# Kernel optimization log

Measured on AMD Instinct MI355X. Metric: run time of the kernel, lower is better.

Reference implementation:

```python
import jax, jax.numpy as jnp
import numpy as np
from jax import lax

EPS = 1e-5      # InstanceNorm2d default eps
SLOPE = 0.2     # LeakyReLU negative slope
K = 3           # kernel size
PAD = 1


def _conv(x, w, pad=PAD):
    # x: [B,C,H,W], w: [O,I,K,K], stride 1
    return lax.conv_general_dilated(x, w, (1, 1), [(pad, pad), (pad, pad)],
                                    dimension_numbers=('NCHW', 'OIHW', 'NCHW'))


def _instance_norm(x, gamma, beta):
    mu = jnp.mean(x, (2, 3), keepdims=True)
    var = jnp.mean((x - mu) ** 2, (2, 3), keepdims=True)
    xn = (x - mu) * lax.rsqrt(var + EPS)
    return xn * gamma[None, :, None, None] + beta[None, :, None, None]


def _lrelu(x):
    return jnp.where(x >= 0, x, SLOPE * x)


def _deform_conv(x, w_off, b_off, w_def):
    # DCNv2: offsets+mask predicted by a 3x3 conv, then modulated bilinear sampling.
    B, C, H, W = x.shape
    om = _conv(x, w_off) + b_off[None, :, None, None]       # [B, 3*K*K, H, W]
    o1, o2, m = jnp.split(om, 3, axis=1)                    # each [B, K*K, H, W]
    off = jnp.concatenate([o1, o2], axis=1)                 # [B, 2*K*K, H, W]
    dy = off[:, 0::2]                                       # [B, K*K, H, W] y-offsets
    dx = off[:, 1::2]                                       # [B, K*K, H, W] x-offsets
    mask = jax.nn.sigmoid(m)                                # [B, K*K, H, W]

    ky = jnp.repeat(jnp.arange(K), K).astype(x.dtype)       # tap row index per k
    kx = jnp.tile(jnp.arange(K), K).astype(x.dtype)         # tap col index per k
    py = dy + jnp.arange(H, dtype=x.dtype)[None, None, :, None] - PAD + ky[None, :, None, None]
    px = dx + jnp.arange(W, dtype=x.dtype)[None, None, None, :] - PAD + kx[None, :, None, None]

    y0 = jnp.floor(py); x0 = jnp.floor(px)
    ly = py - y0; lx = px - x0
    y0i = y0.astype(jnp.int32); x0i = x0.astype(jnp.int32)

    xf = x.reshape(B, C, H * W)

    def gather(iy, ix):
        valid = ((iy >= 0) & (iy < H) & (ix >= 0) & (ix < W)).astype(x.dtype)
        idx = jnp.clip(iy, 0, H - 1) * W + jnp.clip(ix, 0, W - 1)
        v = jax.vmap(lambda f, i: jnp.take(f, i, axis=-1))(xf, idx)  # [B,C,K*K,H,W]
        return v * valid[:, None]

    samp = (gather(y0i, x0i)         * ((1 - ly) * (1 - lx))[:, None]
          + gather(y0i, x0i + 1)     * ((1 - ly) * lx)[:, None]
          + gather(y0i + 1, x0i)     * (ly * (1 - lx))[:, None]
          + gather(y0i + 1, x0i + 1) * (ly * lx)[:, None])          # [B,C,K*K,H,W]

    wk = w_def.reshape(w_def.shape[0], C, K * K)            # [O,C,K*K]
    return jnp.einsum('ock,bckhw,bkhw->bohw', wk, samp, mask)


def setup_inputs() -> dict:
    key = jax.random.key(0)
    ks = jax.random.split(key, 10)
    B, C, H, W = 4, 128, 96, 96
    x = jax.random.normal(ks[0], (B, C, H, W), jnp.float32)
    g1 = 1.0 + 0.05 * jax.random.normal(ks[1], (C,), jnp.float32)
    b1 = 0.05 * jax.random.normal(ks[2], (C,), jnp.float32)
    g2 = 1.0 + 0.05 * jax.random.normal(ks[3], (C,), jnp.float32)
    b2 = 0.05 * jax.random.normal(ks[4], (C,), jnp.float32)
    w1 = jax.random.normal(ks[5], (C, C, K, K), jnp.float32) * 0.03
    bc1 = 0.01 * jax.random.normal(ks[6], (C,), jnp.float32)
    # offset/mask conv: zero-init in the original; use small random values so the
    # irregular bilinear-sampling path is actually exercised.
    w_off = jax.random.normal(ks[7], (3 * K * K, C, K, K), jnp.float32) * 0.01
    b_off = 0.01 * jax.random.normal(ks[8], (3 * K * K,), jnp.float32)
    w_def = jax.random.normal(ks[9], (C, C, K, K), jnp.float32) * 0.03  # DeformConv has bias=None
    return {"x": x, "g1": g1, "b1": b1, "g2": g2, "b2": b2,
            "w1": w1, "bc1": bc1, "w_off": w_off, "b_off": b_off, "w_def": w_def}


def reference(x, g1, b1, g2, b2, w1, bc1, w_off, b_off, w_def):
    h = _lrelu(_instance_norm(x, g1, b1))
    h = _conv(h, w1) + bc1[None, :, None, None]
    h = _lrelu(_instance_norm(h, g2, b2))
    h = _deform_conv(h, w_off, b_off, w_def)
    return h + x
```

## Files before the change

kernel.cpp:

```cpp
#include <hip/hip_runtime.h>
#include <hip/hip_fp16.h>
#include <math.h>

#define HWN 9216
#define HD 96
#define WD 96

typedef _Float16 h8v __attribute__((ext_vector_type(8)));
typedef float f16x16 __attribute__((ext_vector_type(16)));

__device__ __forceinline__ ushort f2h(float f) {
  return __half_as_ushort(__float2half(f));
}
__device__ __forceinline__ __half2 u2h(unsigned u) {
  return __builtin_bit_cast(__half2, u);
}
__device__ __forceinline__ unsigned h2u(__half2 h) {
  return __builtin_bit_cast(unsigned, h);
}
__device__ __forceinline__ h8v u4h(uint4 v) {
  return __builtin_bit_cast(h8v, v);
}
__device__ __forceinline__ f16x16 mfma32(h8v a, h8v b, f16x16 c) {
  return __builtin_amdgcn_mfma_f32_32x32x16_f16(a, b, c, 0, 0, 0);
}
__device__ __forceinline__ __half2 pkmax2(__half2 a, __half2 b) {
  unsigned r;
  asm("v_pk_max_f16 %0, %1, %2" : "=v"(r) : "v"(h2u(a)), "v"(h2u(b)));
  return u2h(r);
}
__device__ __forceinline__ __half2 lrelu2(__half2 v, __half2 c02) {
  return pkmax2(v, __hmul2(v, c02));
}

__global__ __launch_bounds__(256) void packxt_kernel(
    const float* __restrict__ w1, const float* __restrict__ wdef,
    const float* __restrict__ woff, const float* __restrict__ x,
    ushort* __restrict__ w1p, ushort* __restrict__ wdp, ushort* __restrict__ wofp,
    unsigned* __restrict__ xh, float* __restrict__ partS, float* __restrict__ partQ) {
  __shared__ float tl[128][97];
  int bid = blockIdx.x;
  int t = threadIdx.x;
  if (bid < 162) {
    int i = bid * 256 + t;
    const float* src;
    ushort* dst;
    int CT, CO_real, fi;
    if (i < 18432) { src = w1; dst = w1p; CT = 4; CO_real = 128; fi = i; }
    else if (i < 36864) { src = wdef; dst = wdp; CT = 4; CO_real = 128; fi = i - 18432; }
    else { src = woff; dst = wofp; CT = 1; CO_real = 27; fi = i - 36864; }
    int lane = fi & 63;
    int j = fi >> 6;
    int ks = j & 7; j >>= 3;
    int ct = j % CT;
    int kk = j / CT;
    int co = ct * 32 + (lane & 31);
    int c0 = ks * 16 + (lane >> 5) * 8;
    ushort fr[8];
#pragma unroll
    for (int e = 0; e < 8; ++e) {
      float v = 0.f;
      if (co < CO_real) v = src[(size_t)(co * 128 + c0 + e) * 9 + kk];
      fr[e] = f2h(v);
    }
    uint4 o4;
    o4.x = (unsigned)fr[0] | ((unsigned)fr[1] << 16);
    o4.y = (unsigned)fr[2] | ((unsigned)fr[3] << 16);
    o4.z = (unsigned)fr[4] | ((unsigned)fr[5] << 16);
    o4.w = (unsigned)fr[6] | ((unsigned)fr[7] << 16);
    *(uint4*)(dst + (size_t)fi * 8) = o4;
    return;
  }
  int xb = bid - 162;
  int b = xb / 96, y = xb % 96;
  const float* sbase = x + (size_t)b * 128 * HWN + y * WD;
  for (int i = t; i < 3072; i += 256) {
    int c = i / 24, j = i - c * 24;
    const float4 v = *(const float4*)(sbase + (size_t)c * HWN + j * 4);
    tl[c][j * 4 + 0] = v.x;
    tl[c][j * 4 + 1] = v.y;
    tl[c][j * 4 + 2] = v.z;
    tl[c][j * 4 + 3] = v.w;
  }
  __syncthreads();
  {
    int c = t >> 1, half = t & 1;
    float S = 0.f, Q = 0.f;
    for (int j = 0; j < 48; ++j) {
      float v = tl[c][half * 48 + j];
      S += v;
      Q += v * v;
    }
    S += __shfl_xor(S, 1, 64);
    Q += __shfl_xor(Q, 1, 64);
    if (half == 0) {
      partS[((size_t)(b * 96 + y)) * 128 + c] = S;
      partQ[((size_t)(b * 96 + y)) * 128 + c] = Q;
    }
  }
  unsigned* dbase = xh + (size_t)(b * 96 + y) * 96 * 64;
  for (int i = t; i < 6144; i += 256) {
    int xx = i >> 6, c2 = i & 63;
    unsigned lo = f2h(tl[2 * c2][xx]);
    unsigned hi = f2h(tl[2 * c2 + 1][xx]);
    dbase[xx * 64 + c2] = lo | (hi << 16);
  }
}

__global__ __launch_bounds__(64) void finalize_kernel(
    const float* __restrict__ partS, const float* __restrict__ partQ,
    const float* __restrict__ gamma, const float* __restrict__ beta,
    float* __restrict__ sa_, float* __restrict__ sb_, int ntiles) {
  int bc = blockIdx.x;
  int b = bc >> 7, c = bc & 127;
  float S = 0.f, Q = 0.f;
  for (int tl = threadIdx.x; tl < ntiles; tl += 64) {
    S += partS[((size_t)b * ntiles + tl) * 128 + c];
    Q += partQ[((size_t)b * ntiles + tl) * 128 + c];
  }
#pragma unroll
  for (int off = 32; off > 0; off >>= 1) {
    S += __shfl_down(S, off, 64);
    Q += __shfl_down(Q, off, 64);
  }
  if (threadIdx.x == 0) {
    float mu = S / (float)HWN;
    float var = Q / (float)HWN - mu * mu;
    float rs = rsqrtf(var + 1e-5f);
    float a = rs * gamma[c];
    sa_[bc] = a;
    sb_[bc] = beta[c] - mu * a;
  }
}

__global__ __launch_bounds__(256) void stats2_kernel(
    const ushort* __restrict__ hBh, float* __restrict__ partS,
    float* __restrict__ partQ) {
  int tile = blockIdx.x;
  int b = blockIdx.y;
  int t = threadIdx.x;
  int cc = t & 15, pp = t >> 4;
  int wid = t >> 6, lane = t & 63;
  const ushort* base = hBh + ((size_t)b * HWN + tile * 144) * 128 + cc * 8;
  float S[8], Q[8];
#pragma unroll
  for (int e = 0; e < 8; ++e) { S[e] = 0.f; Q[e] = 0.f; }
  for (int i = 0; i < 9; ++i) {
    int pix = i * 16 + pp;
    uint4 v = *(const uint4*)(base + (size_t)pix * 128);
    unsigned ar[4] = {v.x, v.y, v.z, v.w};
#pragma unroll
    for (int j = 0; j < 4; ++j) {
      float2 f = __half22float2(u2h(ar[j]));
      S[2 * j] += f.x; Q[2 * j] += f.x * f.x;
      S[2 * j + 1] += f.y; Q[2 * j + 1] += f.y * f.y;
    }
  }
#pragma unroll
  for (int e = 0; e < 8; ++e) {
    S[e] += __shfl_xor(S[e], 16, 64); Q[e] += __shfl_xor(Q[e], 16, 64);
    S[e] += __shfl_xor(S[e], 32, 64); Q[e] += __shfl_xor(Q[e], 32, 64);
  }
  __shared__ float red[2][4][16][8];
  if (lane < 16) {
#pragma unroll
    for (int e = 0; e < 8; ++e) { red[0][wid][lane][e] = S[e]; red[1][wid][lane][e] = Q[e]; }
  }
  __syncthreads();
  if (t < 16) {
#pragma unroll
    for (int e = 0; e < 8; ++e) {
      float s = red[0][0][t][e] + red[0][1][t][e] + red[0][2][t][e] + red[0][3][t][e];
      float q = red[1][0][t][e] + red[1][1][t][e] + red[1][2][t][e] + red[1][3][t][e];
      partS[((size_t)b * 64 + tile) * 128 + t * 8 + e] = s;
      partQ[((size_t)b * 64 + tile) * 128 + t * 8 + e] = q;
    }
  }
}

__global__ __launch_bounds__(512) void conv1_mfma(
    const ushort* __restrict__ inp, const float* __restrict__ sa_,
    const float* __restrict__ sb_, const ushort* __restrict__ wp,
    const float* __restrict__ bias, ushort* __restrict__ outh) {
  __shared__ ushort halo[100 * 128];
  __shared__ __half2 sah[64], sbh[64];
  int b = blockIdx.y;
  int tile = blockIdx.x;
  int Y0 = (tile / 12) * 8, X0 = (tile % 12) * 8;
  int t = threadIdx.x;
  int lane = t & 63, w = t >> 6;
  if (t < 64) {
    sah[t] = __floats2half2_rn(sa_[b * 128 + 2 * t], sa_[b * 128 + 2 * t + 1]);
    sbh[t] = __floats2half2_rn(sb_[b * 128 + 2 * t], sb_[b * 128 + 2 * t + 1]);
  }
  __syncthreads();
  const __half2 c02 = __float2half2_rn(0.2f);
  const ushort* ib = inp + (size_t)b * HWN * 128;
  for (int i = t; i < 400; i += 512) {
    int r = i >> 2, q = i & 3;
    int gy = Y0 - 1 + r / 10, gx = X0 - 1 + r % 10;
    bool inb = ((unsigned)gy < 96u) && ((unsigned)gx < 96u);
    const uint4* gp4 = (const uint4*)(ib + (size_t)(gy * 96 + gx) * 128 + q * 32);
#pragma unroll
    for (int cc = 0; cc < 4; ++cc) {
      uint4 v = make_uint4(0, 0, 0, 0);
      if (inb) {
        uint4 g = gp4[cc];
        unsigned ar[4] = {g.x, g.y, g.z, g.w};
        int c2b = (q * 4 + cc) * 4;
#pragma unroll
        for (int j = 0; j < 4; ++j) {
          __half2 hv = __hfma2(u2h(ar[j]), sah[c2b + j], sbh[c2b + j]);
          hv = lrelu2(hv, c02);
          ar[j] = h2u(hv);
        }
        v.x = ar[0]; v.y = ar[1]; v.z = ar[2]; v.w = ar[3];
      }
      int ch = (q * 4 + cc) ^ (r & 7);
      *(uint4*)&halo[r * 128 + ch * 8] = v;
    }
  }
  __syncthreads();

  int ct = w >> 1, pt = w & 1;
  int pl = lane & 31, kh = lane >> 5;
  int p = pt * 32 + pl;
  f16x16 acc = (f16x16)(0.f);

  uint4 Acur[8], Anxt[8];
#pragma unroll
  for (int ks = 0; ks < 8; ++ks)
    Acur[ks] = *(const uint4*)(wp + (size_t)((0 * 4 + ct) * 8 + ks) * 512 + lane * 8);

  for (int kk = 0; kk < 9; ++kk) {
    if (kk < 8) {
#pragma unroll
      for (int ks = 0; ks < 8; ++ks)
        Anxt[ks] = *(const uint4*)(wp + (size_t)(((kk + 1) * 4 + ct) * 8 + ks) * 512 + lane * 8);
    }
    int ky = kk / 3, kx = kk % 3;
    int r = ((p >> 3) + ky) * 10 + (p & 7) + kx;
    __builtin_amdgcn_s_setprio(1);
#pragma unroll
    for (int ks = 0; ks < 8; ++ks) {
      int u = (ks * 2 + kh) ^ (r & 7);
      h8v bf = *(const h8v*)&halo[r * 128 + u * 8];
      acc = mfma32(u4h(Acur[ks]), bf, acc);
    }
    __builtin_amdgcn_s_setprio(0);
    if (kk < 8) {
#pragma unroll
      for (int ks = 0; ks < 8; ++ks) Acur[ks] = Anxt[ks];
    }
  }
  int gp = (Y0 + (p >> 3)) * 96 + X0 + (p & 7);
#pragma unroll
  for (int g = 0; g < 4; ++g) {
    int ch0 = ct * 32 + 4 * kh + 8 * g;
    float v0 = acc[4 * g + 0] + bias[ch0 + 0];
    float v1 = acc[4 * g + 1] + bias[ch0 + 1];
    float v2 = acc[4 * g + 2] + bias[ch0 + 2];
    float v3 = acc[4 * g + 3] + bias[ch0 + 3];
    uint2 o;
    o.x = (unsigned)f2h(v0) | ((unsigned)f2h(v1) << 16);
    o.y = (unsigned)f2h(v2) | ((unsigned)f2h(v3) << 16);
    *(uint2*)&outh[((size_t)b * HWN + gp) * 128 + ch0] = o;
  }
}

__device__ __forceinline__ uint4 gaffine(const ushort* hb, int pix, int cc,
                                         const __half2* sa2v, const __half2* sb2v,
                                         __half2 c02) {
  uint4 g = *(const uint4*)(hb + (size_t)pix * 128 + cc * 8);
  unsigned ar[4] = {g.x, g.y, g.z, g.w};
#pragma unroll
  for (int j = 0; j < 4; ++j) {
    __half2 hv = __hfma2(u2h(ar[j]), sa2v[j], sb2v[j]);
    hv = lrelu2(hv, c02);
    ar[j] = h2u(hv);
  }
  return make_uint4(ar[0], ar[1], ar[2], ar[3]);
}

__global__ __launch_bounds__(256) void deform_fused(
    const ushort* __restrict__ h2n, const float* __restrict__ sa_,
    const float* __restrict__ sb_, const ushort* __restrict__ wofp,
    const float* __restrict__ boff, const ushort* __restrict__ wdp,
    const float* __restrict__ x, float* __restrict__ out) {
  __shared__ __align__(16) ushort halo[96 * 128];
  __shared__ __align__(16) ushort S[2][32 * 128];
  __shared__ __align__(16) ushort4 idxs[9][32];
  __shared__ __align__(16) ushort4 wgtc[9][32];
  __shared__ __half2 sah[64], sbh[64];
  float* pf = (float*)S;
  int bid = blockIdx.x;
  int swz = (bid & 7) * 144 + (bid >> 3);
  int b = swz / 288;
  int tile = swz % 288;
  int Y0 = (tile / 12) * 4, X0 = (tile % 12) * 8;
  int t = threadIdx.x;
  int lane = t & 63, w = t >> 6;
  const ushort* hb = h2n + (size_t)b * HWN * 128;
  if (t < 64) {
    sah[t] = __floats2half2_rn(sa_[b * 128 + 2 * t], sa_[b * 128 + 2 * t + 1]);
    sbh[t] = __floats2half2_rn(sb_[b * 128 + 2 * t], sb_[b * 128 + 2 * t + 1]);
  }
  __syncthreads();
  const __half2 c02 = __float2half2_rn(0.2f);

  for (int i = t; i < 1536; i += 256) {
    int pix = i >> 4, u = i & 15;
    int gy = Y0 - 2 + pix / 12, gx = X0 - 2 + pix % 12;
    uint4 v = make_uint4(0, 0, 0, 0);
    if (((unsigned)gy < 96u) && ((unsigned)gx < 96u)) {
      uint4 g = *(const uint4*)(hb + (size_t)(gy * 96 + gx) * 128 + u * 8);
      unsigned ar[4] = {g.x, g.y, g.z, g.w};
#pragma unroll
      for (int j = 0; j < 4; ++j) {
        __half2 hv = __hfma2(u2h(ar[j]), sah[u * 4 + j], sbh[u * 4 + j]);
        hv = lrelu2(hv, c02);
        ar[j] = h2u(hv);
      }
      v.x = ar[0]; v.y = ar[1]; v.z = ar[2]; v.w = ar[3];
    }
    *(uint4*)&halo[pix * 128 + ((u ^ (pix & 15)) * 8)] = v;
  }
  __syncthreads();

  {
    int pl = lane & 31, kh = lane >> 5;
    int p = pl;
    f16x16 accm = (f16x16)(0.f);
    for (int kk = w; kk < 9; kk += 4) {
      int ky = kk / 3, kx = kk % 3;
      int hp = (1 + (p >> 3) + ky) * 12 + 1 + (p & 7) + kx;
#pragma unroll
      for (int ks = 0; ks < 8; ++ks) {
        uint4 a = *(const uint4*)(wofp + (size_t)(kk * 8 + ks) * 512 + lane * 8);
        int u = (ks * 2 + kh) ^ (hp & 15);
        h8v bf = *(const h8v*)&halo[hp * 128 + u * 8];
        accm = mfma32(u4h(a), bf, accm);
      }
    }
#pragma unroll
    for (int reg = 0; reg < 16; ++reg) {
      int co = 4 * kh + (reg & 3) + 8 * (reg >> 2);
      pf[(w * 32 + co) * 32 + p] = accm[reg];
    }
  }
  __syncthreads();

  for (int i = t; i < 288; i += 256) {
    int k = i >> 5, p = i & 31;
    int yy = Y0 + (p >> 3), xx = X0 + (p & 7);
    int cdy = 2 * k, cdx = 2 * k + 1, cm = 18 + k;
    float dy = pf[(0 * 32 + cdy) * 32 + p] + pf[(1 * 32 + cdy) * 32 + p] +
               pf[(2 * 32 + cdy) * 32 + p] + pf[(3 * 32 + cdy) * 32 + p] + boff[cdy];
    float dx = pf[(0 * 32 + cdx) * 32 + p] + pf[(1 * 32 + cdx) * 32 + p] +
               pf[(2 * 32 + cdx) * 32 + p] + pf[(3 * 32 + cdx) * 32 + p] + boff[cdx];
    float mv = pf[(0 * 32 + cm) * 32 + p] + pf[(1 * 32 + cm) * 32 + p] +
               pf[(2 * 32 + cm) * 32 + p] + pf[(3 * 32 + cm) * 32 + p] + boff[cm];
    float mask = 1.0f / (1.0f + expf(-mv));
    float py = dy + (float)(yy - 1 + (k / 3));
    float px = dx + (float)(xx - 1 + (k % 3));
    float fy = floorf(py), fx = floorf(px);
    float lyf = py - fy, lxf = px - fx;
    int y0 = (int)fy, x0 = (int)fx;
    int y1 = y0 + 1, x1 = x0 + 1;
    bool vy0 = (y0 >= 0) && (y0 < HD);
    bool vy1 = (y1 >= 0) && (y1 < HD);
    bool vx0 = (x0 >= 0) && (x0 < WD);
    bool vx1 = (x1 >= 0) && (x1 < WD);
    int y0c = min(max(y0, 0), HD - 1), y1c = min(max(y1, 0), HD - 1);
    int x0c = min(max(x0, 0), WD - 1), x1c = min(max(x1, 0), WD - 1);
    float w0 = (1.f - lyf) * (1.f - lxf) * ((vy0 && vx0) ? mask : 0.f);
    float w1v = (1.f - lyf) * lxf * ((vy0 && vx1) ? mask : 0.f);
    float w2 = lyf * (1.f - lxf) * ((vy1 && vx0) ? mask : 0.f);
    float w3 = lyf * lxf * ((vy1 && vx1) ? mask : 0.f);
    bool inh = (y0c >= Y0 - 2) && (y1c <= Y0 + 5) && (x0c >= X0 - 2) && (x1c <= X0 + 9);
    ushort4 sidx;
    if (inh) {
      int sy0 = y0c - (Y0 - 2), sy1 = y1c - (Y0 - 2);
      int sx0 = x0c - (X0 - 2), sx1 = x1c - (X0 - 2);
      sidx.x = (ushort)(sy0 * 12 + sx0);
      sidx.y = (ushort)(sy0 * 12 + sx1);
      sidx.z = (ushort)(sy1 * 12 + sx0);
      sidx.w = (ushort)(sy1 * 12 + sx1);
    } else {
      sidx.x = (ushort)((y0c * WD + x0c) | 0x8000);
      sidx.y = (ushort)(y0c * WD + x1c);
      sidx.z = (ushort)(y1c * WD + x0c);
      sidx.w = (ushort)(y1c * WD + x1c);
    }
    idxs[k][p] = sidx;
    ushort4 wc;
    wc.x = f2h(w0); wc.y = f2h(w1v); wc.z = f2h(w2); wc.w = f2h(w3);
    wgtc[k][p] = wc;
  }
  __syncthreads();

  int cc = t & 15;
  int pp = t >> 4;
  int ct = w;
  int pl = lane & 31, kh = lane >> 5;
  int pg = pl;
  f16x16 acc = (f16x16)(0.f);
  __half2 sa2v[4], sb2v[4];
#pragma unroll
  for (int j = 0; j < 4; ++j) { sa2v[j] = sah[cc * 4 + j]; sb2v[j] = sbh[cc * 4 + j]; }

  int gp = (Y0 + (pg >> 3)) * 96 + X0 + (pg & 7);
  float xr[16];
#pragma unroll
  for (int reg = 0; reg < 16; ++reg) {
    int co = ct * 32 + 4 * kh + (reg & 3) + 8 * (reg >> 2);
    xr[reg] = x[(size_t)(b * 128 + co) * HWN + gp];
  }

  uint4 AW[8];
  for (int k = 0; k < 9; ++k) {
    const ushort* wk = wdp + (size_t)k * 16384;
#pragma unroll
    for (int ks = 0; ks < 8; ++ks)
      AW[ks] = *(const uint4*)(wk + (size_t)(ct * 8 + ks) * 512 + lane * 8);
    ushort* Sb_w = S[k & 1];
#pragma unroll
    for (int i2 = 0; i2 < 2; ++i2) {
      int p = pp + 16 * i2;
      ushort4 sidx = idxs[k][p];
      ushort4 wc = wgtc[k][p];
      uint4 C0, C1, C2, C3;
      if (sidx.x & 0x8000u) {
        C0 = gaffine(hb, sidx.x & 0x7fff, cc, sa2v, sb2v, c02);
        C1 = gaffine(hb, sidx.y, cc, sa2v, sb2v, c02);
        C2 = gaffine(hb, sidx.z, cc, sa2v, sb2v, c02);
        C3 = gaffine(hb, sidx.w, cc, sa2v, sb2v, c02);
      } else {
        C0 = *(const uint4*)&halo[sidx.x * 128 + ((cc ^ (sidx.x & 15)) * 8)];
        C1 = *(const uint4*)&halo[sidx.y * 128 + ((cc ^ (sidx.y & 15)) * 8)];
        C2 = *(const uint4*)&halo[sidx.z * 128 + ((cc ^ (sidx.z & 15)) * 8)];
        C3 = *(const uint4*)&halo[sidx.w * 128 + ((cc ^ (sidx.w & 15)) * 8)];
      }
      __half2 a0 = u2h((unsigned)wc.x * 0x10001u);
      __half2 a1 = u2h((unsigned)wc.y * 0x10001u);
      __half2 a2 = u2h((unsigned)wc.z * 0x10001u);
      __half2 a3 = u2h((unsigned)wc.w * 0x10001u);
      __half2 s0 = __hmul2(u2h(C0.x), a0);
      __half2 s1 = __hmul2(u2h(C0.y), a0);
      __half2 s2 = __hmul2(u2h(C0.z), a0);
      __half2 s3 = __hmul2(u2h(C0.w), a0);
      s0 = __hfma2(u2h(C1.x), a1, s0); s1 = __hfma2(u2h(C1.y), a1, s1);
      s2 = __hfma2(u2h(C1.z), a1, s2); s3 = __hfma2(u2h(C1.w), a1, s3);
      s0 = __hfma2(u2h(C2.x), a2, s0); s1 = __hfma2(u2h(C2.y), a2, s1);
      s2 = __hfma2(u2h(C2.z), a2, s2); s3 = __hfma2(u2h(C2.w), a2, s3);
      s0 = __hfma2(u2h(C3.x), a3, s0); s1 = __hfma2(u2h(C3.y), a3, s1);
      s2 = __hfma2(u2h(C3.z), a3, s2); s3 = __hfma2(u2h(C3.w), a3, s3);
      uint4 o4;
      o4.x = h2u(s0); o4.y = h2u(s1); o4.z = h2u(s2); o4.w = h2u(s3);
      *(uint4*)&Sb_w[p * 128 + ((cc ^ (p & 15)) * 8)] = o4;
    }
    asm volatile("s_waitcnt lgkmcnt(0)" ::: "memory");
    __builtin_amdgcn_s_barrier();
    const ushort* Sb = S[k & 1];
    __builtin_amdgcn_s_setprio(1);
#pragma unroll
    for (int ks = 0; ks < 8; ++ks) {
      int u = (ks * 2 + kh) ^ (pg & 15);
      h8v bf = *(const h8v*)&Sb[pg * 128 + u * 8];
      acc = mfma32(u4h(AW[ks]), bf, acc);
    }
    __builtin_amdgcn_s_setprio(0);
  }
#pragma unroll
  for (int reg = 0; reg < 16; ++reg) {
    int co = ct * 32 + 4 * kh + (reg & 3) + 8 * (reg >> 2);
    size_t oi = (size_t)(b * 128 + co) * HWN + gp;
    out[oi] = acc[reg] + xr[reg];
  }
}

extern "C" void kernel_launch(void* const* d_in, const int* in_sizes, int n_in,
                              void* d_out, int out_size, void* d_ws, size_t ws_size,
                              hipStream_t stream) {
  const float* x = (const float*)d_in[0];
  const float* g1 = (const float*)d_in[1];
  const float* b1 = (const float*)d_in[2];
  const float* g2 = (const float*)d_in[3];
  const float* b2 = (const float*)d_in[4];
  const float* w1 = (const float*)d_in[5];
  const float* bc1 = (const float*)d_in[6];
  const float* w_off = (const float*)d_in[7];
  const float* b_off = (const float*)d_in[8];
  const float* w_def = (const float*)d_in[9];
  float* out = (float*)d_out;
  float* ws = (float*)d_ws;

  ushort* w1p = (ushort*)ws;
  ushort* wofp = (ushort*)(ws + 73728);
  ushort* wdp = (ushort*)(ws + 92160);
  float* sa1 = ws + 165888;
  float* sb1 = ws + 166400;
  float* sa2 = ws + 166912;
  float* sb2 = ws + 167424;
  float* partS1 = ws + 167936;
  float* partQ1 = ws + 217088;
  float* partS2 = ws + 266240;
  float* partQ2 = ws + 299008;
  ushort* xh = (ushort*)(ws + 331776);
  ushort* hBh = (ushort*)(ws + 2691072);

  packxt_kernel<<<546, 256, 0, stream>>>(w1, w_def, w_off, x, w1p, wdp, wofp,
                                         (unsigned*)xh, partS1, partQ1);
  finalize_kernel<<<512, 64, 0, stream>>>(partS1, partQ1, g1, b1, sa1, sb1, 96);
  conv1_mfma<<<dim3(144, 4), 512, 0, stream>>>(xh, sa1, sb1, w1p, bc1, hBh);
  stats2_kernel<<<dim3(64, 4), 256, 0, stream>>>(hBh, partS2, partQ2);
  finalize_kernel<<<512, 64, 0, stream>>>(partS2, partQ2, g2, b2, sa2, sb2, 64);
  deform_fused<<<dim3(1152), 256, 0, stream>>>(hBh, sa2, sb2, wofp, b_off, wdp, x, out);
}
```

Measured before the change: 81.12 us.

## Fold instance-norm finalize into stats kernels via last-block atomics; halve conv1 block

Removes the two separate finalize kernel launches. The producer kernels now count finished blocks with an atomic counter, and the last block reduces the partial sums into the scale and shift values, at the cost of one memset and a serial reduction inside that single block. Separately, conv1 now runs 256 threads per block, with each wave computing two 32-pixel tiles that reuse the same weight registers. This halves redundant weight loads but gives fewer waves to hide latency.

```diff
diff --git a/kernel.cpp b/kernel.cpp
--- a/kernel.cpp
+++ b/kernel.cpp
@@ -37,8 +37,11 @@
     const float* __restrict__ w1, const float* __restrict__ wdef,
     const float* __restrict__ woff, const float* __restrict__ x,
     ushort* __restrict__ w1p, ushort* __restrict__ wdp, ushort* __restrict__ wofp,
-    unsigned* __restrict__ xh, float* __restrict__ partS, float* __restrict__ partQ) {
+    unsigned* __restrict__ xh, float* __restrict__ partS, float* __restrict__ partQ,
+    const float* __restrict__ g1, const float* __restrict__ b1,
+    float* __restrict__ sa1, float* __restrict__ sb1, int* __restrict__ cnt) {
   __shared__ float tl[128][97];
+  __shared__ int lastv;
   int bid = blockIdx.x;
   int t = threadIdx.x;
   if (bid < 162) {
@@ -105,42 +108,41 @@
     unsigned hi = f2h(tl[2 * c2 + 1][xx]);
     dbase[xx * 64 + c2] = lo | (hi << 16);
   }
-}
-
-__global__ __launch_bounds__(64) void finalize_kernel(
-    const float* __restrict__ partS, const float* __restrict__ partQ,
-    const float* __restrict__ gamma, const float* __restrict__ beta,
-    float* __restrict__ sa_, float* __restrict__ sb_, int ntiles) {
-  int bc = blockIdx.x;
-  int b = bc >> 7, c = bc & 127;
-  float S = 0.f, Q = 0.f;
-  for (int tl = threadIdx.x; tl < ntiles; tl += 64) {
-    S += partS[((size_t)b * ntiles + tl) * 128 + c];
-    Q += partQ[((size_t)b * ntiles + tl) * 128 + c];
-  }
-#pragma unroll
-  for (int off = 32; off > 0; off >>= 1) {
-    S += __shfl_down(S, off, 64);
-    Q += __shfl_down(Q, off, 64);
-  }
-  if (threadIdx.x == 0) {
-    float mu = S / (float)HWN;
-    float var = Q / (float)HWN - mu * mu;
-    float rs = rsqrtf(var + 1e-5f);
-    float a = rs * gamma[c];
-    sa_[bc] = a;
-    sb_[bc] = beta[c] - mu * a;
+  __threadfence();
+  __syncthreads();
+  if (t == 0) lastv = atomicAdd(cnt, 1);
+  __syncthreads();
+  if (lastv == 383) {
+    __threadfence();
+    for (int id = t; id < 512; id += 256) {
+      int bb = id >> 7, c = id & 127;
+      float S = 0.f, Q = 0.f;
+      for (int yy = 0; yy < 96; ++yy) {
+        S += partS[((size_t)(bb * 96 + yy)) * 128 + c];
+        Q += partQ[((size_t)(bb * 96 + yy)) * 128 + c];
+      }
+      float mu = S / (float)HWN;
+      float var = Q / (float)HWN - mu * mu;
+      float rs = rsqrtf(var + 1e-5f);
+      float a = rs * g1[c];
+      sa1[id] = a;
+      sb1[id] = b1[c] - mu * a;
+    }
   }
 }
 
 __global__ __launch_bounds__(256) void stats2_kernel(
     const ushort* __restrict__ hBh, float* __restrict__ partS,
-    float* __restrict__ partQ) {
+    float* __restrict__ partQ, const float* __restrict__ g2,
+    const float* __restrict__ b2, float* __restrict__ sa2,
+    float* __restrict__ sb2, int* __restrict__ cnt) {
   int tile = blockIdx.x;
   int b = blockIdx.y;
   int t = threadIdx.x;
   int cc = t & 15, pp = t >> 4;
   int wid = t >> 6, lane = t & 63;
+  __shared__ float red[2][4][16][8];
+  __shared__ int lastv;
   const ushort* base = hBh + ((size_t)b * HWN + tile * 144) * 128 + cc * 8;
   float S[8], Q[8];
 #pragma unroll
@@ -161,7 +163,6 @@
     S[e] += __shfl_xor(S[e], 16, 64); Q[e] += __shfl_xor(Q[e], 16, 64);
     S[e] += __shfl_xor(S[e], 32, 64); Q[e] += __shfl_xor(Q[e], 32, 64);
   }
-  __shared__ float red[2][4][16][8];
   if (lane < 16) {
 #pragma unroll
     for (int e = 0; e < 8; ++e) { red[0][wid][lane][e] = S[e]; red[1][wid][lane][e] = Q[e]; }
@@ -176,9 +177,30 @@
       partQ[((size_t)b * 64 + tile) * 128 + t * 8 + e] = q;
     }
   }
-}
-
-__global__ __launch_bounds__(512) void conv1_mfma(
+  __threadfence();
+  __syncthreads();
+  if (t == 0) lastv = atomicAdd(cnt, 1);
+  __syncthreads();
+  if (lastv == 255) {
+    __threadfence();
+    for (int id = t; id < 512; id += 256) {
+      int bb = id >> 7, c = id & 127;
+      float Sv = 0.f, Qv = 0.f;
+      for (int tl = 0; tl < 64; ++tl) {
+        Sv += partS[((size_t)bb * 64 + tl) * 128 + c];
+        Qv += partQ[((size_t)bb * 64 + tl) * 128 + c];
+      }
+      float mu = Sv / (float)HWN;
+      float var = Qv / (float)HWN - mu * mu;
+      float rs = rsqrtf(var + 1e-5f);
+      float a = rs * g2[c];
+      sa2[id] = a;
+      sb2[id] = b2[c] - mu * a;
+    }
+  }
+}
+
+__global__ __launch_bounds__(256) void conv1_mfma(
     const ushort* __restrict__ inp, const float* __restrict__ sa_,
     const float* __restrict__ sb_, const ushort* __restrict__ wp,
     const float* __restrict__ bias, ushort* __restrict__ outh) {
@@ -188,7 +210,7 @@
   int tile = blockIdx.x;
   int Y0 = (tile / 12) * 8, X0 = (tile % 12) * 8;
   int t = threadIdx.x;
-  int lane = t & 63, w = t >> 6;
+  int lane = t & 63, ct = t >> 6;
   if (t < 64) {
     sah[t] = __floats2half2_rn(sa_[b * 128 + 2 * t], sa_[b * 128 + 2 * t + 1]);
     sbh[t] = __floats2half2_rn(sb_[b * 128 + 2 * t], sb_[b * 128 + 2 * t + 1]);
@@ -196,7 +218,7 @@
   __syncthreads();
   const __half2 c02 = __float2half2_rn(0.2f);
   const ushort* ib = inp + (size_t)b * HWN * 128;
-  for (int i = t; i < 400; i += 512) {
+  for (int i = t; i < 400; i += 256) {
     int r = i >> 2, q = i & 3;
     int gy = Y0 - 1 + r / 10, gx = X0 - 1 + r % 10;
     bool inb = ((unsigned)gy < 96u) && ((unsigned)gx < 96u);
@@ -222,10 +244,9 @@
   }
   __syncthreads();
 
-  int ct = w >> 1, pt = w & 1;
   int pl = lane & 31, kh = lane >> 5;
-  int p = pt * 32 + pl;
-  f16x16 acc = (f16x16)(0.f);
+  int p0 = pl, p1 = 32 + pl;
+  f16x16 acc0 = (f16x16)(0.f), acc1 = (f16x16)(0.f);
 
   uint4 Acur[8], Anxt[8];
 #pragma unroll
@@ -239,13 +260,17 @@
         Anxt[ks] = *(const uint4*)(wp + (size_t)(((kk + 1) * 4 + ct) * 8 + ks) * 512 + lane * 8);
     }
     int ky = kk / 3, kx = kk % 3;
-    int r = ((p >> 3) + ky) * 10 + (p & 7) + kx;
+    int r0 = ((p0 >> 3) + ky) * 10 + (p0 & 7) + kx;
+    int r1 = ((p1 >> 3) + ky) * 10 + (p1 & 7) + kx;
     __builtin_amdgcn_s_setprio(1);
 #pragma unroll
     for (int ks = 0; ks < 8; ++ks) {
-      int u = (ks * 2 + kh) ^ (r & 7);
-      h8v bf = *(const h8v*)&halo[r * 128 + u * 8];
-      acc = mfma32(u4h(Acur[ks]), bf, acc);
+      int u0 = (ks * 2 + kh) ^ (r0 & 7);
+      h8v bf0 = *(const h8v*)&halo[r0 * 128 + u0 * 8];
+      acc0 = mfma32(u4h(Acur[ks]), bf0, acc0);
+      int u1 = (ks * 2 + kh) ^ (r1 & 7);
+      h8v bf1 = *(const h8v*)&halo[r1 * 128 + u1 * 8];
+      acc1 = mfma32(u4h(Acur[ks]), bf1, acc1);
     }
     __builtin_amdgcn_s_setprio(0);
     if (kk < 8) {
@@ -253,18 +278,23 @@
       for (int ks = 0; ks < 8; ++ks) Acur[ks] = Anxt[ks];
     }
   }
-  int gp = (Y0 + (p >> 3)) * 96 + X0 + (p & 7);
-#pragma unroll
-  for (int g = 0; g < 4; ++g) {
-    int ch0 = ct * 32 + 4 * kh + 8 * g;
-    float v0 = acc[4 * g + 0] + bias[ch0 + 0];
-    float v1 = acc[4 * g + 1] + bias[ch0 + 1];
-    float v2 = acc[4 * g + 2] + bias[ch0 + 2];
-    float v3 = acc[4 * g + 3] + bias[ch0 + 3];
-    uint2 o;
-    o.x = (unsigned)f2h(v0) | ((unsigned)f2h(v1) << 16);
-    o.y = (unsigned)f2h(v2) | ((unsigned)f2h(v3) << 16);
-    *(uint2*)&outh[((size_t)b * HWN + gp) * 128 + ch0] = o;
+#pragma unroll
+  for (int pt = 0; pt < 2; ++pt) {
+    int p = pt ? p1 : p0;
+    const f16x16& acc = pt ? acc1 : acc0;
+    int gp = (Y0 + (p >> 3)) * 96 + X0 + (p & 7);
+#pragma unroll
+    for (int g = 0; g < 4; ++g) {
+      int ch0 = ct * 32 + 4 * kh + 8 * g;
+      float v0 = acc[4 * g + 0] + bias[ch0 + 0];
+      float v1 = acc[4 * g + 1] + bias[ch0 + 1];
+      float v2 = acc[4 * g + 2] + bias[ch0 + 2];
+      float v3 = acc[4 * g + 3] + bias[ch0 + 3];
+      uint2 o;
+      o.x = (unsigned)f2h(v0) | ((unsigned)f2h(v1) << 16);
+      o.y = (unsigned)f2h(v2) | ((unsigned)f2h(v3) << 16);
+      *(uint2*)&outh[((size_t)b * HWN + gp) * 128 + ch0] = o;
+    }
   }
 }
 
@@ -498,22 +528,24 @@
   ushort* w1p = (ushort*)ws;
   ushort* wofp = (ushort*)(ws + 73728);
   ushort* wdp = (ushort*)(ws + 92160);
-  float* sa1 = ws + 165888;
-  float* sb1 = ws + 166400;
-  float* sa2 = ws + 166912;
-  float* sb2 = ws + 167424;
-  float* partS1 = ws + 167936;
-  float* partQ1 = ws + 217088;
-  float* partS2 = ws + 266240;
-  float* partQ2 = ws + 299008;
-  ushort* xh = (ushort*)(ws + 331776);
-  ushort* hBh = (ushort*)(ws + 2691072);
-
+  int* cnt = (int*)(ws + 165888);
+  float* sa1 = ws + 165892;
+  float* sb1 = ws + 166404;
+  float* sa2 = ws + 166916;
+  float* sb2 = ws + 167428;
+  float* partS1 = ws + 167940;
+  float* partQ1 = ws + 217092;
+  float* partS2 = ws + 266244;
+  float* partQ2 = ws + 299012;
+  ushort* xh = (ushort*)(ws + 331780);
+  ushort* hBh = (ushort*)(ws + 2691076);
+
+  hipMemsetAsync(cnt, 0, 8, stream);
   packxt_kernel<<<546, 256, 0, stream>>>(w1, w_def, w_off, x, w1p, wdp, wofp,
-                                         (unsigned*)xh, partS1, partQ1);
-  finalize_kernel<<<512, 64, 0, stream>>>(partS1, partQ1, g1, b1, sa1, sb1, 96);
-  conv1_mfma<<<dim3(144, 4), 512, 0, stream>>>(xh, sa1, sb1, w1p, bc1, hBh);
-  stats2_kernel<<<dim3(64, 4), 256, 0, stream>>>(hBh, partS2, partQ2);
-  finalize_kernel<<<512, 64, 0, stream>>>(partS2, partQ2, g2, b2, sa2, sb2, 64);
+                                         (unsigned*)xh, partS1, partQ1,
+                                         g1, b1, sa1, sb1, cnt + 0);
+  conv1_mfma<<<dim3(144, 4), 256, 0, stream>>>(xh, sa1, sb1, w1p, bc1, hBh);
+  stats2_kernel<<<dim3(64, 4), 256, 0, stream>>>(hBh, partS2, partQ2, g2, b2,
+                                                 sa2, sb2, cnt + 1);
   deform_fused<<<dim3(1152), 256, 0, stream>>>(hBh, sa2, sb2, wofp, b_off, wdp, x, out);
 }
```

Result: slower. 156.5 us (+92.9%).
